# Kernel optimization log

Hardware: AMD Instinct MI355X
Metric: run time of the kernel (lower is better)

The kernel has to match this reference:

```python
import jax, jax.numpy as jnp
import numpy as np

EPS = 1e-5

def _ln(x, g, b):
    m = x.mean(-1, keepdims=True)
    v = x.var(-1, keepdims=True)
    return (x - m) / jnp.sqrt(v + EPS) * g + b

def _ln_na(x):
    m = x.mean(-1, keepdims=True)
    v = x.var(-1, keepdims=True)
    return (x - m) / jnp.sqrt(v + EPS)

def setup_inputs() -> dict:
    key = jax.random.key(0)
    ks = jax.random.split(key, 12)
    B, J, D, H, E, Z = 128, 4096, 64, 128, 256, 32
    s = 0.05
    return {
        "x": jax.random.normal(ks[0], (B, J), jnp.float32),
        "mask": jax.random.randint(ks[1], (B, J), 0, 2, jnp.int32),
        "feature_embedding": jax.random.normal(ks[2], (J, D), jnp.float32),
        "hW1": jax.random.normal(ks[3], (1 + D, H), jnp.float32) * s,
        "hb1": jnp.zeros((H,), jnp.float32),
        "hg1": jnp.ones((H,), jnp.float32),
        "hbt1": jnp.zeros((H,), jnp.float32),
        "hW2": jax.random.normal(ks[4], (H, D), jnp.float32) * s,
        "hb2": jnp.zeros((D,), jnp.float32),
        "hg2": jnp.ones((D,), jnp.float32),
        "hbt2": jnp.zeros((D,), jnp.float32),
        "eW1": jax.random.normal(ks[5], (D, E), jnp.float32) * s,
        "eb1": jnp.zeros((E,), jnp.float32),
        "eW2": jax.random.normal(ks[6], (E, 2 * Z), jnp.float32) * s,
        "eb2": jnp.zeros((2 * Z,), jnp.float32),
    }

def reference(x, mask, feature_embedding, hW1, hb1, hg1, hbt1, hW2, hb2, hg2, hbt2, eW1, eb1, eW2, eb2):
    B, J = x.shape
    D = feature_embedding.shape[1]
    m = (mask > 0).astype(x.dtype)  # (B, J)
    # per-(b,j) MLP on [x_bj, F_j]; masked entries are zeroed before pooling,
    # which equals the original gather-then-MLP-then-sum over observed entries.
    F = jnp.broadcast_to(feature_embedding[None], (B, J, D))
    h_in = jnp.concatenate([x[..., None], F], axis=-1)        # (B, J, 1+D)
    h = jax.nn.relu(_ln(h_in @ hW1 + hb1, hg1, hbt1))          # (B, J, H)
    h = jax.nn.relu(_ln(h @ hW2 + hb2, hg2, hbt2))             # (B, J, D)
    pooled = jnp.einsum('bjd,bj->bd', h, m)                    # sum over observed
    cnt = jnp.maximum(m.sum(-1, keepdims=True), 1.0)
    c = pooled / cnt                                           # mean pool; zeros if no obs
    # FCLayers (2 layers, LayerNorm w/o affine, ReLU each layer)
    e = jax.nn.relu(_ln_na(c @ eW1 + eb1))                     # (B, E)
    out = jax.nn.relu(_ln_na(e @ eW2 + eb2))                   # (B, 2Z)
    mu, logvar = jnp.split(out, 2, axis=-1)
    return (mu, logvar)
```

## Files before the change

### kernel.cpp

```cpp
#include <hip/hip_runtime.h>
#include <hip/hip_bf16.h>

#define B_  128
#define J_  4096
#define D_  64
#define H_  128
#define E_  256
#define Z_  32

typedef __attribute__((ext_vector_type(8))) short short8;
typedef __attribute__((ext_vector_type(4))) float floatx4;

#define OFF_G      0u
#define OFF_GSTATS 2097152u
#define OFF_SCAL   2162688u
#define OFF_W0C    2162944u
#define OFF_C3     2163456u
#define OFF_W2F    2163968u
#define OFF_POOL   2180352u

#if defined(__has_builtin)
#if __has_builtin(__builtin_amdgcn_cvt_pk_bf16_f32)
#define HAVE_CVT_PK_BF16 1
#endif
#endif

#ifdef HAVE_CVT_PK_BF16
static __device__ __forceinline__ unsigned pk2(float a, float b) {
    return __builtin_bit_cast(unsigned, __builtin_amdgcn_cvt_pk_bf16_f32(a, b));
}
#else
static __device__ __forceinline__ unsigned pk2(float a, float b) {
    __hip_bfloat162 t = __float22bfloat162_rn(make_float2(a, b));
    union { __hip_bfloat162 h; unsigned u; } c; c.h = t; return c.u;
}
#endif

__global__ __launch_bounds__(128) void pre_kernel(
    const float* __restrict__ F, const float* __restrict__ hW1,
    const float* __restrict__ hb1, const float* __restrict__ hg1,
    const float* __restrict__ hbt1, const float* __restrict__ hW2,
    float* __restrict__ Gp, float4* __restrict__ Gstats,
    float* __restrict__ scal, float* __restrict__ w0c, float* __restrict__ c3,
    uint4* __restrict__ w2f, float4* __restrict__ zero4)
{
    __shared__ float red[24];
    const int bid = blockIdx.x;
    const int t = threadIdx.x;

    if (bid > 1024) {
        const int base = (bid - 1025) * 256;
        zero4[base + t]       = make_float4(0.f, 0.f, 0.f, 0.f);
        zero4[base + 128 + t] = make_float4(0.f, 0.f, 0.f, 0.f);
        return;
    }

    if (bid == 1024) {
        const float w0h = hW1[t];
        float s = w0h, q = w0h * w0h;
#pragma unroll
        for (int off = 32; off; off >>= 1) {
            s += __shfl_xor(s, off);
            q += __shfl_xor(q, off);
        }
        if ((t & 63) == 0) { red[(t >> 6) * 2] = s; red[(t >> 6) * 2 + 1] = q; }
        __syncthreads();
        const float mw0  = (red[0] + red[2]) * (1.f / (float)H_);
        const float ew02 = (red[1] + red[3]) * (1.f / (float)H_);
        if (t == 0) { scal[0] = mw0; scal[1] = ew02; }
        w0c[t] = (hW1[t] - mw0) * hg1[t];
        c3[t]  = hbt1[t];

        const int lane = t & 63, half = t >> 6;
        const int quad = lane >> 4, col = lane & 15;
        for (int f = half; f < 16; f += 2) {
            const int kstep = f >> 2, nt = f & 3;
            const int kbase = kstep * 32 + quad * 8;
            const int n = nt * 16 + col;
            unsigned r[4];
#pragma unroll
            for (int p = 0; p < 4; p++)
                r[p] = pk2(hW2[(kbase + 2*p) * D_ + n], hW2[(kbase + 2*p + 1) * D_ + n]);
            w2f[f * 64 + lane] = make_uint4(r[0], r[1], r[2], r[3]);
        }
        return;
    }

    const int j0 = bid * 4;
    const int h  = t;
    const float* f0 = F + (size_t)(j0 + 0) * D_;
    const float* f1 = F + (size_t)(j0 + 1) * D_;
    const float* f2p = F + (size_t)(j0 + 2) * D_;
    const float* f3 = F + (size_t)(j0 + 3) * D_;
    const float bias = hb1[h];
    float a0 = bias, a1 = bias, a2 = bias, a3 = bias;
#pragma unroll
    for (int d = 0; d < D_; d++) {
        const float w = hW1[(d + 1) * H_ + h];
        a0 = fmaf(f0[d], w, a0);
        a1 = fmaf(f1[d], w, a1);
        a2 = fmaf(f2p[d], w, a2);
        a3 = fmaf(f3[d], w, a3);
    }

    const float w0h = hW1[h];
    const float g1h = hg1[h];
    float accs[4] = {a0, a1, a2, a3};
#pragma unroll
    for (int q = 0; q < 4; q++) {
        float s1 = accs[q], s2 = w0h * accs[q], s3 = accs[q] * accs[q];
#pragma unroll
        for (int off = 32; off; off >>= 1) {
            s1 += __shfl_xor(s1, off);
            s2 += __shfl_xor(s2, off);
            s3 += __shfl_xor(s3, off);
        }
        if ((h & 63) == 0) {
            int w = h >> 6;
            red[q*6 + w*3 + 0] = s1; red[q*6 + w*3 + 1] = s2; red[q*6 + w*3 + 2] = s3;
        }
    }
    __syncthreads();
    const float inv = 1.f / (float)H_;
#pragma unroll
    for (int q = 0; q < 4; q++) {
        const float mG = (red[q*6 + 0] + red[q*6 + 3]) * inv;
        if (h == 0)
            Gstats[j0 + q] = make_float4(mG, (red[q*6+1] + red[q*6+4]) * inv,
                                             (red[q*6+2] + red[q*6+5]) * inv, 0.f);
        Gp[(j0 + q) * H_ + h] = (accs[q] - mG) * g1h;
    }
}

#define TPW 2
#define BB  4

__global__ __launch_bounds__(256, 2) void main_kernel(
    const float* __restrict__ x, const int* __restrict__ mask,
    const float* __restrict__ Gp, const float4* __restrict__ Gstats,
    const float* __restrict__ scal,
    const float* __restrict__ w0c, const float* __restrict__ c3,
    const uint4* __restrict__ w2f,
    const float* __restrict__ hb2, const float* __restrict__ hg2,
    const float* __restrict__ hbt2,
    float* __restrict__ pooled)
{
    const int tid  = threadIdx.x;
    const int lane = tid & 63;
    const int wv   = tid >> 6;
    const int quad = lane >> 4;
    const int col  = lane & 15;
    const int b0   = blockIdx.y * BB;

    short8 w2r[16];
#pragma unroll
    for (int f = 0; f < 16; f++) {
        union { uint4 v; short8 s; } c; c.v = w2f[f * 64 + lane];
        w2r[f] = c.s;
    }
    float4 wc[4][2], cc[4][2];
#pragma unroll
    for (int k = 0; k < 4; k++) {
        wc[k][0] = ((const float4*)(w0c + k*32 + quad*8))[0];
        wc[k][1] = ((const float4*)(w0c + k*32 + quad*8))[1];
        cc[k][0] = ((const float4*)(c3  + k*32 + quad*8))[0];
        cc[k][1] = ((const float4*)(c3  + k*32 + quad*8))[1];
    }
    float hb2v[4], g2v[4], bt2v[4];
#pragma unroll
    for (int nt = 0; nt < 4; nt++) {
        hb2v[nt] = hb2[nt*16 + col];
        g2v[nt]  = hg2[nt*16 + col];
        bt2v[nt] = hbt2[nt*16 + col];
    }
    const float mw0s  = scal[0];
    const float ew02s = scal[1];

    float pool[BB][4];
#pragma unroll
    for (int bb = 0; bb < BB; bb++)
#pragma unroll
        for (int nt = 0; nt < 4; nt++) pool[bb][nt] = 0.f;

    for (int t = 0; t < TPW; t++) {
        const int tIdx = (blockIdx.x * 4 + wv) * TPW + t;
        const int j0   = tIdx * 16;
        const int rowA = j0 + col;

        const float4 gs = Gstats[rowA];
        float xv[BB]; int4 mk[BB];
#pragma unroll
        for (int bb = 0; bb < BB; bb++) {
            xv[bb] = x[(size_t)(b0 + bb) * J_ + rowA];
            mk[bb] = *(const int4*)(mask + (size_t)(b0 + bb) * J_ + j0 + quad * 4);
        }
        const float* gpr = Gp + rowA * H_ + quad * 8;
        float4 ga[4][2];
#pragma unroll
        for (int k = 0; k < 4; k++) {
            ga[k][0] = ((const float4*)(gpr + k*32))[0];
            ga[k][1] = ((const float4*)(gpr + k*32))[1];
        }

#pragma unroll
        for (int bb = 0; bb < BB; bb++) {
            const float xA = xv[bb];
            const float mean = fmaf(xA, mw0s, gs.x);
            const float eh2  = fmaf(xA, fmaf(xA, ew02s, 2.f * gs.y), gs.z);
            const float r1   = rsqrtf(fmaf(-mean, mean, eh2) + 1e-5f);

            floatx4 acc[4];
#pragma unroll
            for (int nt = 0; nt < 4; nt++) acc[nt] = (floatx4){0.f, 0.f, 0.f, 0.f};

#pragma unroll
            for (int k = 0; k < 4; k++) {
                const float h0 = fmaxf(0.f, fmaf(fmaf(xA, wc[k][0].x, ga[k][0].x), r1, cc[k][0].x));
                const float h1 = fmaxf(0.f, fmaf(fmaf(xA, wc[k][0].y, ga[k][0].y), r1, cc[k][0].y));
                const float h2 = fmaxf(0.f, fmaf(fmaf(xA, wc[k][0].z, ga[k][0].z), r1, cc[k][0].z));
                const float h3 = fmaxf(0.f, fmaf(fmaf(xA, wc[k][0].w, ga[k][0].w), r1, cc[k][0].w));
                const float h4 = fmaxf(0.f, fmaf(fmaf(xA, wc[k][1].x, ga[k][1].x), r1, cc[k][1].x));
                const float h5 = fmaxf(0.f, fmaf(fmaf(xA, wc[k][1].y, ga[k][1].y), r1, cc[k][1].y));
                const float h6 = fmaxf(0.f, fmaf(fmaf(xA, wc[k][1].z, ga[k][1].z), r1, cc[k][1].z));
                const float h7 = fmaxf(0.f, fmaf(fmaf(xA, wc[k][1].w, ga[k][1].w), r1, cc[k][1].w));
                union { unsigned u[4]; short8 s; } af;
                af.u[0] = pk2(h0, h1);
                af.u[1] = pk2(h2, h3);
                af.u[2] = pk2(h4, h5);
                af.u[3] = pk2(h6, h7);
                acc[0] = __builtin_amdgcn_mfma_f32_16x16x32_bf16(af.s, w2r[k*4+0], acc[0], 0, 0, 0);
                acc[1] = __builtin_amdgcn_mfma_f32_16x16x32_bf16(af.s, w2r[k*4+1], acc[1], 0, 0, 0);
                acc[2] = __builtin_amdgcn_mfma_f32_16x16x32_bf16(af.s, w2r[k*4+2], acc[2], 0, 0, 0);
                acc[3] = __builtin_amdgcn_mfma_f32_16x16x32_bf16(af.s, w2r[k*4+3], acc[3], 0, 0, 0);
            }

            float sa[4], qa[4];
#pragma unroll
            for (int r = 0; r < 4; r++) {
                const float v0 = acc[0][r] + hb2v[0];
                const float v1 = acc[1][r] + hb2v[1];
                const float v2 = acc[2][r] + hb2v[2];
                const float v3 = acc[3][r] + hb2v[3];
                acc[0][r] = v0; acc[1][r] = v1; acc[2][r] = v2; acc[3][r] = v3;
                sa[r] = (v0 + v1) + (v2 + v3);
                qa[r] = fmaf(v0, v0, fmaf(v1, v1, fmaf(v2, v2, v3 * v3)));
            }
#pragma unroll
            for (int m = 1; m < 16; m <<= 1) {
#pragma unroll
                for (int r = 0; r < 4; r++) {
                    sa[r] += __shfl_xor(sa[r], m);
                    qa[r] += __shfl_xor(qa[r], m);
                }
            }
            float mrr[4];
            mrr[0] = (mk[bb].x > 0) ? 1.f : 0.f;
            mrr[1] = (mk[bb].y > 0) ? 1.f : 0.f;
            mrr[2] = (mk[bb].z > 0) ? 1.f : 0.f;
            mrr[3] = (mk[bb].w > 0) ? 1.f : 0.f;
#pragma unroll
            for (int r = 0; r < 4; r++) {
                const float m2 = sa[r] * (1.f / 64.f);
                const float v2 = fmaf(-m2, m2, qa[r] * (1.f / 64.f));
                const float r2 = rsqrtf(v2 + 1e-5f);
#pragma unroll
                for (int nt = 0; nt < 4; nt++) {
                    const float rg  = r2 * g2v[nt];
                    const float off = fmaf(-m2, rg, bt2v[nt]);
                    const float o   = fmaxf(0.f, fmaf(acc[nt][r], rg, off));
                    pool[bb][nt] = fmaf(mrr[r], o, pool[bb][nt]);
                }
            }
        }
    }

#pragma unroll
    for (int m = 16; m < 64; m <<= 1)
#pragma unroll
        for (int bb = 0; bb < BB; bb++)
#pragma unroll
            for (int nt = 0; nt < 4; nt++)
                pool[bb][nt] += __shfl_xor(pool[bb][nt], m);

    if (lane < 16) {
#pragma unroll
        for (int bb = 0; bb < BB; bb++)
#pragma unroll
            for (int nt = 0; nt < 4; nt++)
                atomicAdd(&pooled[(size_t)(b0 + bb) * D_ + nt * 16 + lane], pool[bb][nt]);
    }
}

__global__ __launch_bounds__(256) void final_kernel(
    const float* __restrict__ pooled, const int* __restrict__ mask,
    const float* __restrict__ eW1, const float* __restrict__ eb1,
    const float* __restrict__ eW2, const float* __restrict__ eb2,
    float* __restrict__ out)
{
    __shared__ float c_lds[D_];
    __shared__ float e_lds[E_];
    __shared__ float red[8];
    __shared__ float redc[4];
    const int b = blockIdx.x;
    const int t = threadIdx.x;
    const int lane = t & 63, wid = t >> 6;

    {
        const int4* mrow = (const int4*)(mask + (size_t)b * J_);
        int s = 0;
#pragma unroll
        for (int i = 0; i < 4; i++) {
            const int4 v = mrow[i * 256 + t];
            s += (v.x > 0) + (v.y > 0) + (v.z > 0) + (v.w > 0);
        }
        float fs = (float)s;
#pragma unroll
        for (int off = 32; off; off >>= 1) fs += __shfl_xor(fs, off);
        if (lane == 0) redc[wid] = fs;
    }
    __syncthreads();
    const float cn = fmaxf((redc[0] + redc[1]) + (redc[2] + redc[3]), 1.f);
    if (t < D_) c_lds[t] = pooled[(size_t)b * D_ + t] / cn;
    __syncthreads();

    float acc = eb1[t];
#pragma unroll
    for (int d = 0; d < D_; d++)
        acc = fmaf(c_lds[d], eW1[(size_t)d * E_ + t], acc);

    float s = acc, s2 = acc * acc;
#pragma unroll
    for (int off = 32; off; off >>= 1) {
        s  += __shfl_xor(s, off);
        s2 += __shfl_xor(s2, off);
    }
    if ((t & 63) == 0) { red[wid * 2] = s; red[wid * 2 + 1] = s2; }
    __syncthreads();
    s  = red[0] + red[2] + red[4] + red[6];
    s2 = red[1] + red[3] + red[5] + red[7];
    const float m = s * (1.f / (float)E_);
    const float v = fmaf(-m, m, s2 * (1.f / (float)E_));
    const float r = rsqrtf(v + 1e-5f);
    e_lds[t] = fmaxf(0.f, (acc - m) * r);
    __syncthreads();

    if (t < 64) {
        float a2 = eb2[t];
#pragma unroll 8
        for (int k = 0; k < E_; k++)
            a2 = fmaf(e_lds[k], eW2[(size_t)k * 64 + t], a2);

        float u = a2, u2 = a2 * a2;
#pragma unroll
        for (int off = 32; off; off >>= 1) {
            u  += __shfl_xor(u, off);
            u2 += __shfl_xor(u2, off);
        }
        const float m2 = u * (1.f / 64.f);
        const float v2 = fmaf(-m2, m2, u2 * (1.f / 64.f));
        const float r2 = rsqrtf(v2 + 1e-5f);
        const float o  = fmaxf(0.f, (a2 - m2) * r2);
        if (t < Z_) out[(size_t)b * Z_ + t] = o;
        else        out[(size_t)B_ * Z_ + (size_t)b * Z_ + (t - Z_)] = o;
    }
}

extern "C" void kernel_launch(void* const* d_in, const int* in_sizes, int n_in,
                              void* d_out, int out_size, void* d_ws, size_t ws_size,
                              hipStream_t stream) {
    const float* x    = (const float*)d_in[0];
    const int*   mask = (const int*)d_in[1];
    const float* F    = (const float*)d_in[2];
    const float* hW1  = (const float*)d_in[3];
    const float* hb1  = (const float*)d_in[4];
    const float* hg1  = (const float*)d_in[5];
    const float* hbt1 = (const float*)d_in[6];
    const float* hW2  = (const float*)d_in[7];
    const float* hb2  = (const float*)d_in[8];
    const float* hg2  = (const float*)d_in[9];
    const float* hbt2 = (const float*)d_in[10];
    const float* eW1  = (const float*)d_in[11];
    const float* eb1  = (const float*)d_in[12];
    const float* eW2  = (const float*)d_in[13];
    const float* eb2  = (const float*)d_in[14];
    float* out = (float*)d_out;

    char* ws = (char*)d_ws;
    float*  Gp     = (float*)(ws + OFF_G);
    float4* Gstats = (float4*)(ws + OFF_GSTATS);
    float*  scal   = (float*)(ws + OFF_SCAL);
    float*  w0c    = (float*)(ws + OFF_W0C);
    float*  c3     = (float*)(ws + OFF_C3);
    uint4*  w2f    = (uint4*)(ws + OFF_W2F);
    float*  pooled = (float*)(ws + OFF_POOL);

    pre_kernel<<<1033, 128, 0, stream>>>(F, hW1, hb1, hg1, hbt1, hW2,
                                         Gp, Gstats, scal, w0c, c3, w2f,
                                         (float4*)pooled);
    main_kernel<<<dim3(J_ / (16 * 4 * TPW), B_ / BB), 256, 0, stream>>>(
        x, mask, Gp, Gstats, scal, w0c, c3, w2f, hb2, hg2, hbt2, pooled);
    final_kernel<<<B_, E_, 0, stream>>>(pooled, mask, eW1, eb1, eW2, eb2, out);
}
```

Baseline: 138.0 us.

## Reuse Gp tile across 8 batch rows, use DPP row reductions, pack mask bits

```diff
diff --git a/kernel.cpp b/kernel.cpp
--- a/kernel.cpp
+++ b/kernel.cpp
@@ -35,6 +35,19 @@
     union { __hip_bfloat162 h; unsigned u; } c; c.h = t; return c.u;
 }
 #endif
+
+static __device__ __forceinline__ float row16_sum(float v) {
+    int x;
+    x = __builtin_amdgcn_update_dpp(0, __builtin_bit_cast(int, v), 0xB1,  0xf, 0xf, true);
+    v += __builtin_bit_cast(float, x);
+    x = __builtin_amdgcn_update_dpp(0, __builtin_bit_cast(int, v), 0x4E,  0xf, 0xf, true);
+    v += __builtin_bit_cast(float, x);
+    x = __builtin_amdgcn_update_dpp(0, __builtin_bit_cast(int, v), 0x124, 0xf, 0xf, true);
+    v += __builtin_bit_cast(float, x);
+    x = __builtin_amdgcn_update_dpp(0, __builtin_bit_cast(int, v), 0x128, 0xf, 0xf, true);
+    v += __builtin_bit_cast(float, x);
+    return v;
+}
 
 __global__ __launch_bounds__(128) void pre_kernel(
     const float* __restrict__ F, const float* __restrict__ hW1,
@@ -132,8 +145,7 @@
     }
 }
 
-#define TPW 2
-#define BB  4
+#define BB  8
 
 __global__ __launch_bounds__(256, 2) void main_kernel(
     const float* __restrict__ x, const int* __restrict__ mask,
@@ -176,35 +188,40 @@
     const float mw0s  = scal[0];
     const float ew02s = scal[1];
 
+    const int tIdx = blockIdx.x * 4 + wv;
+    const int j0   = tIdx * 16;
+    const int rowA = j0 + col;
+
+    const float4 gs = Gstats[rowA];
+    const float* gpr = Gp + rowA * H_ + quad * 8;
+    float4 ga[4][2];
+#pragma unroll
+    for (int k = 0; k < 4; k++) {
+        ga[k][0] = ((const float4*)(gpr + k*32))[0];
+        ga[k][1] = ((const float4*)(gpr + k*32))[1];
+    }
+
     float pool[BB][4];
 #pragma unroll
     for (int bb = 0; bb < BB; bb++)
 #pragma unroll
         for (int nt = 0; nt < 4; nt++) pool[bb][nt] = 0.f;
 
-    for (int t = 0; t < TPW; t++) {
-        const int tIdx = (blockIdx.x * 4 + wv) * TPW + t;
-        const int j0   = tIdx * 16;
-        const int rowA = j0 + col;
-
-        const float4 gs = Gstats[rowA];
-        float xv[BB]; int4 mk[BB];
-#pragma unroll
-        for (int bb = 0; bb < BB; bb++) {
-            xv[bb] = x[(size_t)(b0 + bb) * J_ + rowA];
-            mk[bb] = *(const int4*)(mask + (size_t)(b0 + bb) * J_ + j0 + quad * 4);
-        }
-        const float* gpr = Gp + rowA * H_ + quad * 8;
-        float4 ga[4][2];
-#pragma unroll
-        for (int k = 0; k < 4; k++) {
-            ga[k][0] = ((const float4*)(gpr + k*32))[0];
-            ga[k][1] = ((const float4*)(gpr + k*32))[1];
-        }
-
-#pragma unroll
-        for (int bb = 0; bb < BB; bb++) {
-            const float xA = xv[bb];
+#pragma unroll
+    for (int g = 0; g < 2; g++) {
+        float xv[4]; int mp[4];
+#pragma unroll
+        for (int i = 0; i < 4; i++) {
+            const int b = b0 + g * 4 + i;
+            xv[i] = x[(size_t)b * J_ + rowA];
+            const int4 mv = *(const int4*)(mask + (size_t)b * J_ + j0 + quad * 4);
+            mp[i] = (mv.x > 0) | ((mv.y > 0) << 1) | ((mv.z > 0) << 2) | ((mv.w > 0) << 3);
+        }
+
+#pragma unroll
+        for (int i = 0; i < 4; i++) {
+            const int bb = g * 4 + i;
+            const float xA = xv[i];
             const float mean = fmaf(xA, mw0s, gs.x);
             const float eh2  = fmaf(xA, fmaf(xA, ew02s, 2.f * gs.y), gs.z);
             const float r1   = rsqrtf(fmaf(-mean, mean, eh2) + 1e-5f);
@@ -246,20 +263,13 @@
                 qa[r] = fmaf(v0, v0, fmaf(v1, v1, fmaf(v2, v2, v3 * v3)));
             }
 #pragma unroll
-            for (int m = 1; m < 16; m <<= 1) {
-#pragma unroll
-                for (int r = 0; r < 4; r++) {
-                    sa[r] += __shfl_xor(sa[r], m);
-                    qa[r] += __shfl_xor(qa[r], m);
-                }
+            for (int r = 0; r < 4; r++) {
+                sa[r] = row16_sum(sa[r]);
+                qa[r] = row16_sum(qa[r]);
             }
-            float mrr[4];
-            mrr[0] = (mk[bb].x > 0) ? 1.f : 0.f;
-            mrr[1] = (mk[bb].y > 0) ? 1.f : 0.f;
-            mrr[2] = (mk[bb].z > 0) ? 1.f : 0.f;
-            mrr[3] = (mk[bb].w > 0) ? 1.f : 0.f;
 #pragma unroll
             for (int r = 0; r < 4; r++) {
+                const float mrr = (float)((mp[i] >> r) & 1);
                 const float m2 = sa[r] * (1.f / 64.f);
                 const float v2 = fmaf(-m2, m2, qa[r] * (1.f / 64.f));
                 const float r2 = rsqrtf(v2 + 1e-5f);
@@ -268,7 +278,7 @@
                     const float rg  = r2 * g2v[nt];
                     const float off = fmaf(-m2, rg, bt2v[nt]);
                     const float o   = fmaxf(0.f, fmaf(acc[nt][r], rg, off));
-                    pool[bb][nt] = fmaf(mrr[r], o, pool[bb][nt]);
+                    pool[bb][nt] = fmaf(mrr, o, pool[bb][nt]);
                 }
             }
         }
@@ -397,7 +407,7 @@
     pre_kernel<<<1033, 128, 0, stream>>>(F, hW1, hb1, hg1, hbt1, hW2,
                                          Gp, Gstats, scal, w0c, c3, w2f,
                                          (float4*)pooled);
-    main_kernel<<<dim3(J_ / (16 * 4 * TPW), B_ / BB), 256, 0, stream>>>(
+    main_kernel<<<dim3(J_ / (16 * 4), B_ / BB), 256, 0, stream>>>(
         x, mask, Gp, Gstats, scal, w0c, c3, w2f, hb2, hg2, hbt2, pooled);
     final_kernel<<<B_, E_, 0, stream>>>(pooled, mask, eW1, eb1, eW2, eb2, out);
 }
```

New measurement: 146.4 us. +6.1%, slower.

## Fuse final encoder MLP into main kernel via last-block ticket counter

Applied to the files above, without the earlier changes.

```diff
diff --git a/kernel.cpp b/kernel.cpp
--- a/kernel.cpp
+++ b/kernel.cpp
@@ -18,6 +18,7 @@
 #define OFF_C3     2163456u
 #define OFF_W2F    2163968u
 #define OFF_POOL   2180352u
+#define OFF_TICK   2213120u
 
 #if defined(__has_builtin)
 #if __has_builtin(__builtin_amdgcn_cvt_pk_bf16_f32)
@@ -36,13 +37,15 @@
 }
 #endif
 
+
 __global__ __launch_bounds__(128) void pre_kernel(
     const float* __restrict__ F, const float* __restrict__ hW1,
     const float* __restrict__ hb1, const float* __restrict__ hg1,
     const float* __restrict__ hbt1, const float* __restrict__ hW2,
     float* __restrict__ Gp, float4* __restrict__ Gstats,
     float* __restrict__ scal, float* __restrict__ w0c, float* __restrict__ c3,
-    uint4* __restrict__ w2f, float4* __restrict__ zero4)
+    uint4* __restrict__ w2f, float4* __restrict__ zero4,
+    int* __restrict__ tickets)
 {
     __shared__ float red[24];
     const int bid = blockIdx.x;
@@ -56,6 +59,7 @@
     }
 
     if (bid == 1024) {
+        if (t < 32) tickets[t] = 0;
         const float w0h = hW1[t];
         float s = w0h, q = w0h * w0h;
 #pragma unroll
@@ -143,8 +147,17 @@
     const uint4* __restrict__ w2f,
     const float* __restrict__ hb2, const float* __restrict__ hg2,
     const float* __restrict__ hbt2,
-    float* __restrict__ pooled)
+    const float* __restrict__ eW1, const float* __restrict__ eb1,
+    const float* __restrict__ eW2, const float* __restrict__ eb2,
+    float* __restrict__ pooled, int* __restrict__ tickets,
+    float* __restrict__ out)
 {
+    __shared__ float c_lds[D_];
+    __shared__ float e_lds[E_];
+    __shared__ float hred[8];
+    __shared__ float redc[4];
+    __shared__ int   tick_s;
+
     const int tid  = threadIdx.x;
     const int lane = tid & 63;
     const int wv   = tid >> 6;
@@ -289,79 +302,77 @@
             for (int nt = 0; nt < 4; nt++)
                 atomicAdd(&pooled[(size_t)(b0 + bb) * D_ + nt * 16 + lane], pool[bb][nt]);
     }
-}
-
-__global__ __launch_bounds__(256) void final_kernel(
-    const float* __restrict__ pooled, const int* __restrict__ mask,
-    const float* __restrict__ eW1, const float* __restrict__ eb1,
-    const float* __restrict__ eW2, const float* __restrict__ eb2,
-    float* __restrict__ out)
-{
-    __shared__ float c_lds[D_];
-    __shared__ float e_lds[E_];
-    __shared__ float red[8];
-    __shared__ float redc[4];
-    const int b = blockIdx.x;
-    const int t = threadIdx.x;
-    const int lane = t & 63, wid = t >> 6;
-
-    {
-        const int4* mrow = (const int4*)(mask + (size_t)b * J_);
-        int s = 0;
-#pragma unroll
-        for (int i = 0; i < 4; i++) {
-            const int4 v = mrow[i * 256 + t];
-            s += (v.x > 0) + (v.y > 0) + (v.z > 0) + (v.w > 0);
-        }
-        float fs = (float)s;
-#pragma unroll
-        for (int off = 32; off; off >>= 1) fs += __shfl_xor(fs, off);
-        if (lane == 0) redc[wid] = fs;
-    }
+
+    __threadfence();
     __syncthreads();
-    const float cn = fmaxf((redc[0] + redc[1]) + (redc[2] + redc[3]), 1.f);
-    if (t < D_) c_lds[t] = pooled[(size_t)b * D_ + t] / cn;
+    if (tid == 0) tick_s = atomicAdd(&tickets[blockIdx.y], 1);
     __syncthreads();
-
-    float acc = eb1[t];
-#pragma unroll
-    for (int d = 0; d < D_; d++)
-        acc = fmaf(c_lds[d], eW1[(size_t)d * E_ + t], acc);
-
-    float s = acc, s2 = acc * acc;
-#pragma unroll
-    for (int off = 32; off; off >>= 1) {
-        s  += __shfl_xor(s, off);
-        s2 += __shfl_xor(s2, off);
-    }
-    if ((t & 63) == 0) { red[wid * 2] = s; red[wid * 2 + 1] = s2; }
-    __syncthreads();
-    s  = red[0] + red[2] + red[4] + red[6];
-    s2 = red[1] + red[3] + red[5] + red[7];
-    const float m = s * (1.f / (float)E_);
-    const float v = fmaf(-m, m, s2 * (1.f / (float)E_));
-    const float r = rsqrtf(v + 1e-5f);
-    e_lds[t] = fmaxf(0.f, (acc - m) * r);
-    __syncthreads();
-
-    if (t < 64) {
-        float a2 = eb2[t];
+    if (tick_s != 31) return;
+    __threadfence();
+
+    const int wid = tid >> 6;
+    for (int bb = 0; bb < BB; bb++) {
+        const int b = b0 + bb;
+
+        {
+            const int4* mrow = (const int4*)(mask + (size_t)b * J_);
+            int s = 0;
+#pragma unroll
+            for (int i = 0; i < 4; i++) {
+                const int4 v = mrow[i * 256 + tid];
+                s += (v.x > 0) + (v.y > 0) + (v.z > 0) + (v.w > 0);
+            }
+            float fs = (float)s;
+#pragma unroll
+            for (int off = 32; off; off >>= 1) fs += __shfl_xor(fs, off);
+            if (lane == 0) redc[wid] = fs;
+        }
+        __syncthreads();
+        const float cn = fmaxf((redc[0] + redc[1]) + (redc[2] + redc[3]), 1.f);
+        if (tid < D_) c_lds[tid] = atomicAdd(&pooled[(size_t)b * D_ + tid], 0.f) / cn;
+        __syncthreads();
+
+        float acc = eb1[tid];
+#pragma unroll
+        for (int d = 0; d < D_; d++)
+            acc = fmaf(c_lds[d], eW1[(size_t)d * E_ + tid], acc);
+
+        float s = acc, s2 = acc * acc;
+#pragma unroll
+        for (int off = 32; off; off >>= 1) {
+            s  += __shfl_xor(s, off);
+            s2 += __shfl_xor(s2, off);
+        }
+        if ((tid & 63) == 0) { hred[wid * 2] = s; hred[wid * 2 + 1] = s2; }
+        __syncthreads();
+        s  = hred[0] + hred[2] + hred[4] + hred[6];
+        s2 = hred[1] + hred[3] + hred[5] + hred[7];
+        const float m = s * (1.f / (float)E_);
+        const float v = fmaf(-m, m, s2 * (1.f / (float)E_));
+        const float r = rsqrtf(v + 1e-5f);
+        e_lds[tid] = fmaxf(0.f, (acc - m) * r);
+        __syncthreads();
+
+        if (tid < 64) {
+            float a2 = eb2[tid];
 #pragma unroll 8
-        for (int k = 0; k < E_; k++)
-            a2 = fmaf(e_lds[k], eW2[(size_t)k * 64 + t], a2);
-
-        float u = a2, u2 = a2 * a2;
-#pragma unroll
-        for (int off = 32; off; off >>= 1) {
-            u  += __shfl_xor(u, off);
-            u2 += __shfl_xor(u2, off);
-        }
-        const float m2 = u * (1.f / 64.f);
-        const float v2 = fmaf(-m2, m2, u2 * (1.f / 64.f));
-        const float r2 = rsqrtf(v2 + 1e-5f);
-        const float o  = fmaxf(0.f, (a2 - m2) * r2);
-        if (t < Z_) out[(size_t)b * Z_ + t] = o;
-        else        out[(size_t)B_ * Z_ + (size_t)b * Z_ + (t - Z_)] = o;
+            for (int k = 0; k < E_; k++)
+                a2 = fmaf(e_lds[k], eW2[(size_t)k * 64 + tid], a2);
+
+            float u = a2, u2 = a2 * a2;
+#pragma unroll
+            for (int off = 32; off; off >>= 1) {
+                u  += __shfl_xor(u, off);
+                u2 += __shfl_xor(u2, off);
+            }
+            const float m2 = u * (1.f / 64.f);
+            const float v2 = fmaf(-m2, m2, u2 * (1.f / 64.f));
+            const float r2 = rsqrtf(v2 + 1e-5f);
+            const float o  = fmaxf(0.f, (a2 - m2) * r2);
+            if (tid < Z_) out[(size_t)b * Z_ + tid] = o;
+            else          out[(size_t)B_ * Z_ + (size_t)b * Z_ + (tid - Z_)] = o;
+        }
+        __syncthreads();
     }
 }
 
@@ -393,11 +404,12 @@
     float*  c3     = (float*)(ws + OFF_C3);
     uint4*  w2f    = (uint4*)(ws + OFF_W2F);
     float*  pooled = (float*)(ws + OFF_POOL);
+    int*    tick   = (int*)(ws + OFF_TICK);
 
     pre_kernel<<<1033, 128, 0, stream>>>(F, hW1, hb1, hg1, hbt1, hW2,
                                          Gp, Gstats, scal, w0c, c3, w2f,
-                                         (float4*)pooled);
+                                         (float4*)pooled, tick);
     main_kernel<<<dim3(J_ / (16 * 4 * TPW), B_ / BB), 256, 0, stream>>>(
-        x, mask, Gp, Gstats, scal, w0c, c3, w2f, hb2, hg2, hbt2, pooled);
-    final_kernel<<<B_, E_, 0, stream>>>(pooled, mask, eW1, eb1, eW2, eb2, out);
+        x, mask, Gp, Gstats, scal, w0c, c3, w2f, hb2, hg2, hbt2,
+        eW1, eb1, eW2, eb2, pooled, tick, out);
 }
```

After: 204.8 us. 1.48x slower.
